# Performance work log

Measured on AMD Instinct MI355X. Metric: run time of the kernel, lower is better.

## Reference

```python
import jax, jax.numpy as jnp
import numpy as np

B, F0, D = 2048, 40, 32
LAYER0, LAYER1 = 128, 128  # layer_size=(128,128), split_half=True -> field_nums=[40,64]


def setup_inputs() -> dict:
    key = jax.random.key(0)
    k1, k2, k3 = jax.random.split(key, 3)
    x = jax.random.normal(k1, (B, F0, D), dtype=jnp.float32)
    # TF conv1d filters: [1, F_prev*F0, size]; we store them reshaped [F0, F_prev_fields, size]
    # Layer 0: F_prev = F0 = 40 -> W0 flattened index m = i*F0 + j, i over x0 fields, j over hidden fields
    W0 = jax.random.normal(k2, (F0, F0, LAYER0), dtype=jnp.float32) * 0.05
    b0 = jnp.zeros((LAYER0,), dtype=jnp.float32)
    # Layer 1: F_prev = LAYER0 // 2 = 64 (split_half)
    W1 = jax.random.normal(k3, (F0, LAYER0 // 2, LAYER1), dtype=jnp.float32) * 0.05
    b1 = jnp.zeros((LAYER1,), dtype=jnp.float32)
    return {"x": x, "W0": W0, "b0": b0, "W1": W1, "b1": b1}


def reference(x, W0, b0, W1, b1):
    # CIN layer 0: outer product x0 (x) x0 over fields per embedding dim, then 1x1 conv + bias + relu
    # TF flattens dot_result as index i*F_prev + j, matching W0[i, j, s].
    h0 = jax.nn.relu(jnp.einsum('bid,bjd,ijs->bsd', x, x, W0) + b0[None, :, None])  # (B, 128, D)
    half = LAYER0 // 2
    next_hidden, direct0 = h0[:, :half, :], h0[:, half:, :]  # split_half
    # CIN layer 1 (last layer): all feature maps go to direct connect
    direct1 = jax.nn.relu(
        jnp.einsum('bid,bjd,ijs->bsd', x, next_hidden, W1) + b1[None, :, None]
    )  # (B, 128, D)
    result = jnp.concatenate([direct0, direct1], axis=1)  # (B, 192, D)
    return jnp.sum(result, axis=-1)  # (B, 192)
```

## Files before the change

kernel.cpp:

```cpp
#include <hip/hip_runtime.h>
#include <stdint.h>


typedef __attribute__((ext_vector_type(8))) _Float16 half8;
typedef __attribute__((ext_vector_type(2))) _Float16 half2v;
typedef __attribute__((ext_vector_type(4))) float f32x4;

__device__ __forceinline__ unsigned short f2h(float f) {
    return __builtin_bit_cast(unsigned short, (_Float16)f);
}
__device__ __forceinline__ float qsum(float v) {
    v += __shfl_xor(v, 16, 64);
    v += __shfl_xor(v, 32, 64);
    return v;
}
__device__ __forceinline__ void gl_lds16(const unsigned short* g, unsigned short* l) {
    __builtin_amdgcn_global_load_lds(
        (const __attribute__((address_space(1))) unsigned int*)g,
        (__attribute__((address_space(3))) unsigned int*)l,
        16, 0, 0);
}

__global__ void permute_w_both(const float* __restrict__ W0, const float* __restrict__ W1,
                               unsigned short* __restrict__ Wp0, unsigned short* __restrict__ Wp1)
{
    int t = blockIdx.x;
    int s = threadIdx.x >> 1, h = threadIdx.x & 1;
    const float* W; unsigned short* Wp; int JW, tt;
    if (t < 50) { W = W0; Wp = Wp0; JW = 40; tt = t; }
    else        { W = W1; Wp = Wp1; JW = 64; tt = t - 50; }
    int jc = tt / 10, ic = tt - jc * 10;
    unsigned short outv[16];
    #pragma unroll
    for (int q = 0; q < 16; ++q) {
        int kl = h * 16 + q;
        int i = ic * 4 + (kl >> 3), j = jc * 8 + (kl & 7);
        outv[q] = f2h(W[((size_t)(i * JW + j)) * 128 + s]);
    }
    unsigned short* dst = Wp + (size_t)tt * 4096 + s * 32 + h * 16;
    *(uint4*)dst       = *(const uint4*)outv;
    *(uint4*)(dst + 8) = *(const uint4*)(outv + 8);
}

#define WBUF 20480

template<int NJC>
__device__ __forceinline__ void gemm_phase(
    const unsigned short* __restrict__ Wp,
    const unsigned short* __restrict__ Jl,
    int jstride,
    const unsigned int xi2[4][10],
    unsigned short* Wb,
    f32x4 acc[4][4], int tid)
{
    constexpr int T = NJC * 10;
    const int lane = tid & 63;
    const int wv = tid >> 6;
    const int rt = wv & 3;
    const int sh = tid >> 8;
    const int ml = lane & 15;
    const int kc = lane >> 4;

    const unsigned short* jrow[4];
    #pragma unroll
    for (int mt = 0; mt < 4; ++mt)
        jrow[mt] = Jl + (rt * 64 + mt * 16 + ml) * jstride;

    const unsigned short* brd = Wb + (sh * 64 + ml) * 32 + kc * 8;
    const unsigned short* gsrc = Wp + tid * 8;
    unsigned short* ldst = Wb + wv * 512;

    auto stage_period = [&](int buf, int t0) {
        #pragma unroll
        for (int u = 0; u < 5; ++u)
            gl_lds16(gsrc + (size_t)(t0 + u) * 4096, ldst + buf * WBUF + u * 4096);
    };

    stage_period(0, 0);
    __syncthreads();

    for (int jc2 = 0; jc2 < NJC; ++jc2) {
        uint4 jv[4];
        #pragma unroll
        for (int mt = 0; mt < 4; ++mt) jv[mt] = *(const uint4*)(jrow[mt] + jc2 * 8);

        #pragma unroll
        for (int half = 0; half < 2; ++half) {
            const int p  = jc2 * 2 + half;
            const int cb = p & 1;
            const int nb = cb ^ 1;
            if ((p + 1) * 5 < T) stage_period(nb, (p + 1) * 5);
            #pragma unroll
            for (int u = 0; u < 5; ++u) {
                const int ic = half * 5 + u;
                uint4 bv[4];
                #pragma unroll
                for (int nt = 0; nt < 4; ++nt)
                    bv[nt] = *(const uint4*)(brd + cb * WBUF + u * 4096 + nt * 512);
                uint4 av[4];
                #pragma unroll
                for (int mt = 0; mt < 4; ++mt) {
                    half2v x2 = __builtin_bit_cast(half2v, xi2[mt][ic]);
                    av[mt].x = __builtin_bit_cast(unsigned int,
                        (half2v)(x2 * __builtin_bit_cast(half2v, jv[mt].x)));
                    av[mt].y = __builtin_bit_cast(unsigned int,
                        (half2v)(x2 * __builtin_bit_cast(half2v, jv[mt].y)));
                    av[mt].z = __builtin_bit_cast(unsigned int,
                        (half2v)(x2 * __builtin_bit_cast(half2v, jv[mt].z)));
                    av[mt].w = __builtin_bit_cast(unsigned int,
                        (half2v)(x2 * __builtin_bit_cast(half2v, jv[mt].w)));
                }
                #pragma unroll
                for (int mt = 0; mt < 4; ++mt)
                    #pragma unroll
                    for (int nt = 0; nt < 4; ++nt)
                        acc[mt][nt] = __builtin_amdgcn_mfma_f32_16x16x32_f16(
                            __builtin_bit_cast(half8, av[mt]),
                            __builtin_bit_cast(half8, bv[nt]),
                            acc[mt][nt], 0, 0, 0);
            }
            __syncthreads();
        }
    }
}

__global__ __launch_bounds__(512, 2)
void fused_two_layer(const float* __restrict__ x,
                     const unsigned short* __restrict__ W0p,
                     const float* __restrict__ b0,
                     const unsigned short* __restrict__ W1p,
                     const float* __restrict__ b1,
                     float* __restrict__ out)
{
    __shared__ __align__(16) unsigned short Xl[256 * 40];
    __shared__ __align__(16) unsigned short NH[256 * 72];
    __shared__ __align__(16) unsigned short Wb[2 * WBUF];

    const int tid  = threadIdx.x;
    const int lane = tid & 63;
    const int rt   = (tid >> 6) & 3;
    const int sh   = tid >> 8;
    const int ml   = lane & 15;
    const int kc   = lane >> 4;

    const float* xblk = x + (size_t)blockIdx.x * (8 * 40 * 32);
    #pragma unroll
    for (int bl = 0; bl < 8; ++bl) {
        #pragma unroll
        for (int k = 0; k < 3; ++k) {
            int f = 512 * k + tid;
            if (f < 1280) {
                int i = f >> 5, d = f & 31;
                Xl[(bl * 32 + d) * 40 + i] = f2h(xblk[bl * 1280 + f]);
            }
        }
    }
    __syncthreads();

    unsigned int xi2[4][10];
    #pragma unroll
    for (int mt = 0; mt < 4; ++mt) {
        const unsigned short* xr = Xl + (rt * 64 + mt * 16 + ml) * 40;
        #pragma unroll
        for (int ic = 0; ic < 10; ++ic) {
            unsigned int u = xr[ic * 4 + kc];
            xi2[mt][ic] = u | (u << 16);
        }
    }

    f32x4 acc[4][4];
    const f32x4 zero4 = {0.f, 0.f, 0.f, 0.f};
    #pragma unroll
    for (int mt = 0; mt < 4; ++mt)
        #pragma unroll
        for (int nt = 0; nt < 4; ++nt) acc[mt][nt] = zero4;

    gemm_phase<5>(W0p, Xl, 40, xi2, Wb, acc, tid);

    {
        float bias[4];
        #pragma unroll
        for (int nt = 0; nt < 4; ++nt) bias[nt] = b0[sh * 64 + nt * 16 + ml];
        if (sh == 0) {
            #pragma unroll
            for (int mt = 0; mt < 4; ++mt) {
                int r = rt * 64 + mt * 16 + (kc << 2);
                #pragma unroll
                for (int nt = 0; nt < 4; ++nt) {
                    int s = nt * 16 + ml;
                    #pragma unroll
                    for (int rg = 0; rg < 4; ++rg) {
                        float v = fmaxf(acc[mt][nt][rg] + bias[nt], 0.0f);
                        NH[(r + rg) * 72 + s] = f2h(v);
                    }
                }
            }
        } else {
            int bb = blockIdx.x * 8 + rt * 2;
            #pragma unroll
            for (int nt = 0; nt < 4; ++nt) {
                float sA = 0.f, sB = 0.f;
                #pragma unroll
                for (int rg = 0; rg < 4; ++rg) {
                    sA += fmaxf(acc[0][nt][rg] + bias[nt], 0.f) + fmaxf(acc[1][nt][rg] + bias[nt], 0.f);
                    sB += fmaxf(acc[2][nt][rg] + bias[nt], 0.f) + fmaxf(acc[3][nt][rg] + bias[nt], 0.f);
                }
                sA = qsum(sA); sB = qsum(sB);
                if (lane < 16) {
                    int col = nt * 16 + lane;
                    out[(size_t)bb * 192 + col]       = sA;
                    out[(size_t)(bb + 1) * 192 + col] = sB;
                }
            }
        }
    }
    __syncthreads();

    #pragma unroll
    for (int mt = 0; mt < 4; ++mt)
        #pragma unroll
        for (int nt = 0; nt < 4; ++nt) acc[mt][nt] = zero4;

    gemm_phase<8>(W1p, NH, 72, xi2, Wb, acc, tid);

    {
        float bias[4];
        #pragma unroll
        for (int nt = 0; nt < 4; ++nt) bias[nt] = b1[sh * 64 + nt * 16 + ml];
        int bb = blockIdx.x * 8 + rt * 2;
        #pragma unroll
        for (int nt = 0; nt < 4; ++nt) {
            float sA = 0.f, sB = 0.f;
            #pragma unroll
            for (int rg = 0; rg < 4; ++rg) {
                sA += fmaxf(acc[0][nt][rg] + bias[nt], 0.f) + fmaxf(acc[1][nt][rg] + bias[nt], 0.f);
                sB += fmaxf(acc[2][nt][rg] + bias[nt], 0.f) + fmaxf(acc[3][nt][rg] + bias[nt], 0.f);
            }
            sA = qsum(sA); sB = qsum(sB);
            if (lane < 16) {
                int col = 64 + sh * 64 + nt * 16 + lane;
                out[(size_t)bb * 192 + col]       = sA;
                out[(size_t)(bb + 1) * 192 + col] = sB;
            }
        }
    }
}

extern "C" void kernel_launch(void* const* d_in, const int* in_sizes, int n_in,
                              void* d_out, int out_size, void* d_ws, size_t ws_size,
                              hipStream_t stream) {
    const float* x  = (const float*)d_in[0];
    const float* W0 = (const float*)d_in[1];
    const float* b0 = (const float*)d_in[2];
    const float* W1 = (const float*)d_in[3];
    const float* b1 = (const float*)d_in[4];
    float* out = (float*)d_out;

    unsigned short* W0p = (unsigned short*)d_ws;
    unsigned short* W1p = (unsigned short*)((char*)d_ws + 50 * 4096 * 2);

    permute_w_both<<<130, 256, 0, stream>>>(W0, W1, W0p, W1p);
    fused_two_layer<<<256, 512, 0, stream>>>(x, W0p, b0, W1p, b1, out);
}
```

Before: 123.6 us.

## Exploit symmetry of layer-0 outer product to skip lower-triangle tiles

Layer 0 computes x_i*x_j, which is symmetric, so the weight permute step folds W0[i,j]+W0[j,i] into upper-triangle entries and keeps only the tiles with i<=j. This cuts layer-0 MFMA tiles from 50 to 30. The GEMM loop is rebuilt around a flat tile schedule that reloads the j-row operand only when the j-chunk changes. The weights are also permuted into an MFMA-lane-linear layout so the LDS B-reads index simply by lane. Summing two fp16-rounded weights adds a small precision change.

```diff
diff --git a/kernel.cpp b/kernel.cpp
--- a/kernel.cpp
+++ b/kernel.cpp
@@ -5,6 +5,18 @@
 typedef __attribute__((ext_vector_type(8))) _Float16 half8;
 typedef __attribute__((ext_vector_type(2))) _Float16 half2v;
 typedef __attribute__((ext_vector_type(4))) float f32x4;
+
+#define T0 30
+#define T1 80
+#define WBUF 20480
+
+__host__ __device__ constexpr int ic0_of(int t) {
+    return (t < 2) ? t : (t < 6) ? (t - 2) : (t < 12) ? (t - 6)
+         : (t < 20) ? (t - 12) : (t - 20);
+}
+__host__ __device__ constexpr int jc0_of(int t) {
+    return (t < 2) ? 0 : (t < 6) ? 1 : (t < 12) ? 2 : (t < 20) ? 3 : 4;
+}
 
 __device__ __forceinline__ unsigned short f2h(float f) {
     return __builtin_bit_cast(unsigned short, (_Float16)f);
@@ -24,27 +36,45 @@
 __global__ void permute_w_both(const float* __restrict__ W0, const float* __restrict__ W1,
                                unsigned short* __restrict__ Wp0, unsigned short* __restrict__ Wp1)
 {
-    int t = blockIdx.x;
-    int s = threadIdx.x >> 1, h = threadIdx.x & 1;
-    const float* W; unsigned short* Wp; int JW, tt;
-    if (t < 50) { W = W0; Wp = Wp0; JW = 40; tt = t; }
-    else        { W = W1; Wp = Wp1; JW = 64; tt = t - 50; }
-    int jc = tt / 10, ic = tt - jc * 10;
+    const int t = blockIdx.x;
+    const int tid = threadIdx.x;
     unsigned short outv[16];
-    #pragma unroll
-    for (int q = 0; q < 16; ++q) {
-        int kl = h * 16 + q;
-        int i = ic * 4 + (kl >> 3), j = jc * 8 + (kl & 7);
-        outv[q] = f2h(W[((size_t)(i * JW + j)) * 128 + s]);
-    }
-    unsigned short* dst = Wp + (size_t)tt * 4096 + s * 32 + h * 16;
+    unsigned short* dst;
+    if (t < T0) {
+        const int ic = ic0_of(t), jc = jc0_of(t);
+        #pragma unroll
+        for (int q = 0; q < 16; ++q) {
+            int pos  = tid * 16 + q;
+            int oc   = pos & 7, lane = (pos >> 3) & 63;
+            int nt   = (pos >> 9) & 3, sh = pos >> 11;
+            int s    = sh * 64 + nt * 16 + (lane & 15);
+            int i    = ic * 4 + (lane >> 4), j = jc * 8 + oc;
+            float v = 0.0f;
+            if (i < j)       v = W0[((size_t)(i * 40 + j)) * 128 + s]
+                               + W0[((size_t)(j * 40 + i)) * 128 + s];
+            else if (i == j) v = W0[((size_t)(i * 40 + i)) * 128 + s];
+            outv[q] = f2h(v);
+        }
+        dst = Wp0 + (size_t)t * 4096 + tid * 16;
+    } else {
+        const int tt = t - T0;
+        const int jc = tt / 10, ic = tt % 10;
+        #pragma unroll
+        for (int q = 0; q < 16; ++q) {
+            int pos  = tid * 16 + q;
+            int oc   = pos & 7, lane = (pos >> 3) & 63;
+            int nt   = (pos >> 9) & 3, sh = pos >> 11;
+            int s    = sh * 64 + nt * 16 + (lane & 15);
+            int i    = ic * 4 + (lane >> 4), j = jc * 8 + oc;
+            outv[q] = f2h(W1[((size_t)(i * 64 + j)) * 128 + s]);
+        }
+        dst = Wp1 + (size_t)tt * 4096 + tid * 16;
+    }
     *(uint4*)dst       = *(const uint4*)outv;
     *(uint4*)(dst + 8) = *(const uint4*)(outv + 8);
 }
 
-#define WBUF 20480
-
-template<int NJC>
+template<int T, int PHASE>
 __device__ __forceinline__ void gemm_phase(
     const unsigned short* __restrict__ Wp,
     const unsigned short* __restrict__ Jl,
@@ -53,20 +83,18 @@
     unsigned short* Wb,
     f32x4 acc[4][4], int tid)
 {
-    constexpr int T = NJC * 10;
     const int lane = tid & 63;
     const int wv = tid >> 6;
     const int rt = wv & 3;
     const int sh = tid >> 8;
     const int ml = lane & 15;
-    const int kc = lane >> 4;
 
     const unsigned short* jrow[4];
     #pragma unroll
     for (int mt = 0; mt < 4; ++mt)
         jrow[mt] = Jl + (rt * 64 + mt * 16 + ml) * jstride;
 
-    const unsigned short* brd = Wb + (sh * 64 + ml) * 32 + kc * 8;
+    const unsigned short* brd = Wb + sh * 2048 + lane * 8;
     const unsigned short* gsrc = Wp + tid * 8;
     unsigned short* ldst = Wb + wv * 512;
 
@@ -79,48 +107,52 @@
     stage_period(0, 0);
     __syncthreads();
 
-    for (int jc2 = 0; jc2 < NJC; ++jc2) {
-        uint4 jv[4];
-        #pragma unroll
-        for (int mt = 0; mt < 4; ++mt) jv[mt] = *(const uint4*)(jrow[mt] + jc2 * 8);
-
-        #pragma unroll
-        for (int half = 0; half < 2; ++half) {
-            const int p  = jc2 * 2 + half;
-            const int cb = p & 1;
-            const int nb = cb ^ 1;
-            if ((p + 1) * 5 < T) stage_period(nb, (p + 1) * 5);
-            #pragma unroll
-            for (int u = 0; u < 5; ++u) {
-                const int ic = half * 5 + u;
-                uint4 bv[4];
+    uint4 jv[4];
+    constexpr int NP = T / 5;
+    #pragma unroll
+    for (int p = 0; p < NP; ++p) {
+        const int cb = p & 1;
+        const int nb = cb ^ 1;
+        if ((p + 1) * 5 < T) stage_period(nb, (p + 1) * 5);
+        #pragma unroll
+        for (int u = 0; u < 5; ++u) {
+            const int t  = p * 5 + u;
+            const int ic = (PHASE == 0) ? ic0_of(t) : (t % 10);
+            const int jc = (PHASE == 0) ? jc0_of(t) : (t / 10);
+            const bool rl = (t == 0) ||
+                (jc != ((PHASE == 0) ? jc0_of(t - 1) : ((t - 1) / 10)));
+            if (rl) {
+                #pragma unroll
+                for (int mt = 0; mt < 4; ++mt)
+                    jv[mt] = *(const uint4*)(jrow[mt] + jc * 8);
+            }
+            uint4 bv[4];
+            #pragma unroll
+            for (int nt = 0; nt < 4; ++nt)
+                bv[nt] = *(const uint4*)(brd + cb * WBUF + u * 4096 + nt * 512);
+            uint4 av[4];
+            #pragma unroll
+            for (int mt = 0; mt < 4; ++mt) {
+                half2v x2 = __builtin_bit_cast(half2v, xi2[mt][ic]);
+                av[mt].x = __builtin_bit_cast(unsigned int,
+                    (half2v)(x2 * __builtin_bit_cast(half2v, jv[mt].x)));
+                av[mt].y = __builtin_bit_cast(unsigned int,
+                    (half2v)(x2 * __builtin_bit_cast(half2v, jv[mt].y)));
+                av[mt].z = __builtin_bit_cast(unsigned int,
+                    (half2v)(x2 * __builtin_bit_cast(half2v, jv[mt].z)));
+                av[mt].w = __builtin_bit_cast(unsigned int,
+                    (half2v)(x2 * __builtin_bit_cast(half2v, jv[mt].w)));
+            }
+            #pragma unroll
+            for (int mt = 0; mt < 4; ++mt)
                 #pragma unroll
                 for (int nt = 0; nt < 4; ++nt)
-                    bv[nt] = *(const uint4*)(brd + cb * WBUF + u * 4096 + nt * 512);
-                uint4 av[4];
-                #pragma unroll
-                for (int mt = 0; mt < 4; ++mt) {
-                    half2v x2 = __builtin_bit_cast(half2v, xi2[mt][ic]);
-                    av[mt].x = __builtin_bit_cast(unsigned int,
-                        (half2v)(x2 * __builtin_bit_cast(half2v, jv[mt].x)));
-                    av[mt].y = __builtin_bit_cast(unsigned int,
-                        (half2v)(x2 * __builtin_bit_cast(half2v, jv[mt].y)));
-                    av[mt].z = __builtin_bit_cast(unsigned int,
-                        (half2v)(x2 * __builtin_bit_cast(half2v, jv[mt].z)));
-                    av[mt].w = __builtin_bit_cast(unsigned int,
-                        (half2v)(x2 * __builtin_bit_cast(half2v, jv[mt].w)));
-                }
-                #pragma unroll
-                for (int mt = 0; mt < 4; ++mt)
-                    #pragma unroll
-                    for (int nt = 0; nt < 4; ++nt)
-                        acc[mt][nt] = __builtin_amdgcn_mfma_f32_16x16x32_f16(
-                            __builtin_bit_cast(half8, av[mt]),
-                            __builtin_bit_cast(half8, bv[nt]),
-                            acc[mt][nt], 0, 0, 0);
-            }
-            __syncthreads();
-        }
+                    acc[mt][nt] = __builtin_amdgcn_mfma_f32_16x16x32_f16(
+                        __builtin_bit_cast(half8, av[mt]),
+                        __builtin_bit_cast(half8, bv[nt]),
+                        acc[mt][nt], 0, 0, 0);
+        }
+        __syncthreads();
     }
 }
 
@@ -175,7 +207,7 @@
         #pragma unroll
         for (int nt = 0; nt < 4; ++nt) acc[mt][nt] = zero4;
 
-    gemm_phase<5>(W0p, Xl, 40, xi2, Wb, acc, tid);
+    gemm_phase<T0, 0>(W0p, Xl, 40, xi2, Wb, acc, tid);
 
     {
         float bias[4];
@@ -221,7 +253,7 @@
         #pragma unroll
         for (int nt = 0; nt < 4; ++nt) acc[mt][nt] = zero4;
 
-    gemm_phase<8>(W1p, NH, 72, xi2, Wb, acc, tid);
+    gemm_phase<T1, 1>(W1p, NH, 72, xi2, Wb, acc, tid);
 
     {
         float bias[4];
@@ -257,8 +289,8 @@
     float* out = (float*)d_out;
 
     unsigned short* W0p = (unsigned short*)d_ws;
-    unsigned short* W1p = (unsigned short*)((char*)d_ws + 50 * 4096 * 2);
-
-    permute_w_both<<<130, 256, 0, stream>>>(W0, W1, W0p, W1p);
+    unsigned short* W1p = (unsigned short*)((char*)d_ws + T0 * 4096 * 2);
+
+    permute_w_both<<<T0 + T1, 256, 0, stream>>>(W0, W1, W0p, W1p);
     fused_two_layer<<<256, 512, 0, stream>>>(x, W0p, b0, W1p, b1, out);
 }
```

New measurement: 117.7 us. 4.7% less time.
